# Kernel tuning notes

Measured on AMD Instinct MI355X. Metric: run time of the kernel, lower is better.

## Reference

```python
import jax, jax.numpy as jnp
import numpy as np

N = 50000      # nodes
E = 800000     # edges (avg degree 16)
DIN = 128
DOUT = 64
ALPHA = 0.5    # DirGATConv mixing coefficient
NEG_SLOPE = 0.2  # PyG GATConv default negative_slope


def setup_inputs() -> dict:
    key = jax.random.key(0)
    ks = jax.random.split(key, 12)
    x = jax.random.normal(ks[0], (N, DIN), jnp.float32)
    edge_index = jax.random.randint(ks[1], (2, E), 0, N, dtype=jnp.int64)

    def p(k, shape):
        return jax.random.normal(k, shape, jnp.float32) * 0.05

    return dict(
        x=x,
        edge_index=edge_index,
        W1=p(ks[2], (DIN, DOUT)), att_src1=p(ks[3], (DOUT,)), att_dst1=p(ks[4], (DOUT,)), b1=jnp.zeros((DOUT,), jnp.float32),
        W2=p(ks[5], (DIN, DOUT)), att_src2=p(ks[6], (DOUT,)), att_dst2=p(ks[7], (DOUT,)), b2=jnp.zeros((DOUT,), jnp.float32),
    )


def _gat_conv(x, src, dst, W, a_src, a_dst, b):
    """PyG GATConv with heads=1: linear, per-dst softmax attention, scatter-add."""
    n = x.shape[0]
    loops = jnp.arange(n, dtype=src.dtype)
    src = jnp.concatenate([src, loops])  # add_self_loops=True (PyG default)
    dst = jnp.concatenate([dst, loops])

    xw = x @ W                                # [N, DOUT]
    a_s = xw @ a_src                          # [N]  per-node src attention score
    a_d = xw @ a_dst                          # [N]  per-node dst attention score
    e = jax.nn.leaky_relu(a_s[src] + a_d[dst], NEG_SLOPE)  # [E+N]

    # numerically-stable softmax over edges grouped by destination node
    m = jax.ops.segment_max(e, dst, num_segments=n)
    m = jnp.where(jnp.isfinite(m), m, 0.0)    # nodes w/o in-edges -> safe value
    ex = jnp.exp(e - m[dst])
    denom = jax.ops.segment_sum(ex, dst, num_segments=n)
    coef = ex / (denom[dst] + 1e-16)          # [E+N]

    out = jax.ops.segment_sum(coef[:, None] * xw[src], dst, num_segments=n)
    return out + b


def reference(x, edge_index, W1, att_src1, att_dst1, b1, W2, att_src2, att_dst2, b2):
    src, dst = edge_index[0], edge_index[1]
    out_fwd = _gat_conv(x, src, dst, W1, att_src1, att_dst1, b1)   # src -> dst
    out_rev = _gat_conv(x, dst, src, W2, att_src2, att_dst2, b2)   # dst -> src (transposed edges)
    return (1.0 - ALPHA) * out_fwd + ALPHA * out_rev
```

## Files before the change

kernel.cpp:

```cpp
#include <hip/hip_runtime.h>

#define DIN 128
#define DOUT 64
#define NEG_SLOPE 0.2f
#define ALPHA 0.5f
#define NBUK 512
#define EPB  4096
#define CAP  4608
#define BCCAP 6144

typedef __attribute__((ext_vector_type(8))) short bf16x8;
typedef __attribute__((ext_vector_type(4))) float f32x4;

__device__ __forceinline__ float lrelu(float x) { return x > 0.0f ? x : NEG_SLOPE * x; }

__device__ __forceinline__ unsigned short f2bf(float f) {
    unsigned u = __float_as_uint(f);
    unsigned r = (u + 0x7fffu + ((u >> 16) & 1u)) >> 16;
    return (unsigned short)r;
}
__device__ __forceinline__ float bf2f(unsigned short h) {
    return __uint_as_float((unsigned)h << 16);
}
__device__ __forceinline__ float readlane_f(float v, int l) {
    return __int_as_float(__builtin_amdgcn_readlane(__float_as_int(v), l));
}

__device__ __forceinline__ void dev_wfrag(
    const float* __restrict__ W1, const float* __restrict__ W2,
    unsigned short* __restrict__ wf, int blk, int tid)
{
    int combo = blk * 4 + (tid >> 6);
    int mat = combo >> 4;
    int kk = (combo >> 2) & 3;
    int t = combo & 3;
    int l = tid & 63;
    int g = l >> 4, c = l & 15;
    const float* W = mat ? W2 : W1;
    #pragma unroll
    for (int j = 0; j < 8; ++j) {
        float w = W[(kk * 32 + g * 8 + j) * DOUT + t * 16 + c];
        wf[(size_t)((mat * 16 + kk * 4 + t) * 512) + l * 8 + j] = f2bf(w);
    }
}

__device__ __forceinline__ void dev_proj(
    const float* __restrict__ x, const unsigned short* __restrict__ wf,
    const float* __restrict__ as1, const float* __restrict__ ad1,
    const float* __restrict__ as2, const float* __restrict__ ad2,
    unsigned short* __restrict__ xw1, unsigned short* __restrict__ xw2,
    float* __restrict__ s1, float* __restrict__ d1,
    float* __restrict__ s2, float* __restrict__ d2, int n, int projblk, int tid)
{
    int ntiles = (n + 15) >> 4;
    int tbase = projblk * 8 + (tid >> 6) * 2;
    if (tbase >= ntiles) return;
    int l = tid & 63;
    int g = l >> 4, c = l & 15;

    bf16x8 ah[2][4];
    #pragma unroll
    for (int u = 0; u < 2; ++u) {
        int arow = (tbase + u) * 16 + c;
        if (arow >= n) arow = n - 1;
        const float* xr = x + (size_t)arow * DIN + g * 8;
        #pragma unroll
        for (int kk = 0; kk < 4; ++kk) {
            float4 v0 = *(const float4*)(xr + kk * 32);
            float4 v1 = *(const float4*)(xr + kk * 32 + 4);
            float xv[8] = {v0.x, v0.y, v0.z, v0.w, v1.x, v1.y, v1.z, v1.w};
            #pragma unroll
            for (int j = 0; j < 8; ++j) ah[u][kk][j] = (short)f2bf(xv[j]);
        }
    }

    float vs1[2][4] = {}, vd1[2][4] = {}, vs2[2][4] = {}, vd2[2][4] = {};
    const bf16x8* wfv = (const bf16x8*)wf;

    #pragma unroll
    for (int t = 0; t < 4; ++t) {
        f32x4 C1[2] = {{0.f,0.f,0.f,0.f},{0.f,0.f,0.f,0.f}};
        f32x4 C2[2] = {{0.f,0.f,0.f,0.f},{0.f,0.f,0.f,0.f}};
        #pragma unroll
        for (int kk = 0; kk < 4; ++kk) {
            bf16x8 bh1 = wfv[(size_t)((0 * 16 + kk * 4 + t) * 64) + l];
            bf16x8 bh2 = wfv[(size_t)((1 * 16 + kk * 4 + t) * 64) + l];
            #pragma unroll
            for (int u = 0; u < 2; ++u) {
                C1[u] = __builtin_amdgcn_mfma_f32_16x16x32_bf16(ah[u][kk], bh1, C1[u], 0, 0, 0);
                C2[u] = __builtin_amdgcn_mfma_f32_16x16x32_bf16(ah[u][kk], bh2, C2[u], 0, 0, 0);
            }
        }
        float a1v = as1[t * 16 + c], a2v = ad1[t * 16 + c];
        float a3v = as2[t * 16 + c], a4v = ad2[t * 16 + c];
        #pragma unroll
        for (int u = 0; u < 2; ++u) {
            #pragma unroll
            for (int r = 0; r < 4; ++r) {
                vs1[u][r] = fmaf(C1[u][r], a1v, vs1[u][r]);
                vd1[u][r] = fmaf(C1[u][r], a2v, vd1[u][r]);
                vs2[u][r] = fmaf(C2[u][r], a3v, vs2[u][r]);
                vd2[u][r] = fmaf(C2[u][r], a4v, vd2[u][r]);
                int node = (tbase + u) * 16 + g * 4 + r;
                if (node < n) {
                    xw1[(size_t)node * DOUT + t * 16 + c] = f2bf(C1[u][r]);
                    xw2[(size_t)node * DOUT + t * 16 + c] = f2bf(C2[u][r]);
                }
            }
        }
    }
    #pragma unroll
    for (int off = 1; off < 16; off <<= 1) {
        #pragma unroll
        for (int u = 0; u < 2; ++u) {
            #pragma unroll
            for (int r = 0; r < 4; ++r) {
                vs1[u][r] += __shfl_xor(vs1[u][r], off);
                vd1[u][r] += __shfl_xor(vd1[u][r], off);
                vs2[u][r] += __shfl_xor(vs2[u][r], off);
                vd2[u][r] += __shfl_xor(vd2[u][r], off);
            }
        }
    }
    if (c == 0) {
        #pragma unroll
        for (int u = 0; u < 2; ++u) {
            #pragma unroll
            for (int r = 0; r < 4; ++r) {
                int node = (tbase + u) * 16 + g * 4 + r;
                if (node < n) {
                    s1[node] = vs1[u][r]; d1[node] = vd1[u][r];
                    s2[node] = vs2[u][r]; d2[node] = vd2[u][r];
                }
            }
        }
    }
}

__global__ __launch_bounds__(256) void fusedA_kernel(
    const float* __restrict__ W1, const float* __restrict__ W2,
    unsigned short* __restrict__ wf,
    const int* __restrict__ src, const int* __restrict__ dst,
    int* __restrict__ bkcur, unsigned* __restrict__ staging,
    int e, int n, int nblk)
{
    __shared__ int cnt[NBUK];
    int blk = blockIdx.x, tid = threadIdx.x;
    if (blk >= nblk) { dev_wfrag(W1, W2, wf, blk - nblk, tid); return; }

    for (int b = tid; b < NBUK; b += 256) cnt[b] = 0;
    __syncthreads();
    int base = blk * EPB;
    for (int k = 0; k < EPB / 256; ++k) {
        int t = base + k * 256 + tid;
        if (t < e) {
            atomicAdd(&cnt[dst[t] >> 8], 1);
            atomicAdd(&cnt[(n + src[t]) >> 8], 1);
        }
    }
    __syncthreads();
    for (int b = tid; b < NBUK; b += 256) {
        int c = cnt[b];
        cnt[b] = c ? atomicAdd(&bkcur[b], c) : 0;
    }
    __syncthreads();
    for (int k = 0; k < EPB / 256; ++k) {
        int t = base + k * 256 + tid;
        if (t < e) {
            int s = src[t], d = dst[t];
            int bF = d >> 8;
            int pF = atomicAdd(&cnt[bF], 1);
            if (pF < CAP)
                staging[(size_t)bF * CAP + pF] = ((unsigned)(d & 255) << 16) | (unsigned)s;
            int segR = n + s;
            int bR = segR >> 8;
            int pR = atomicAdd(&cnt[bR], 1);
            if (pR < CAP)
                staging[(size_t)bR * CAP + pR] = ((unsigned)(segR & 255) << 16) | (unsigned)d;
        }
    }
}

__global__ __launch_bounds__(256) void fusedB_kernel(
    const int* __restrict__ bkcur, const unsigned* __restrict__ staging,
    int* __restrict__ csr, int* __restrict__ offs,
    int n2, int e2, int nbuk_eff,
    const float* __restrict__ x, const unsigned short* __restrict__ wf,
    const float* __restrict__ as1, const float* __restrict__ ad1,
    const float* __restrict__ as2, const float* __restrict__ ad2,
    unsigned short* __restrict__ xw1, unsigned short* __restrict__ xw2,
    float* __restrict__ s1, float* __restrict__ d1,
    float* __restrict__ s2, float* __restrict__ d2, int n)
{
    __shared__ int cb[NBUK];
    __shared__ int sc[256];
    __shared__ int segcnt[256];
    __shared__ int segoff[256];
    __shared__ unsigned cache[BCCAP];
    int blk = blockIdx.x, tid = threadIdx.x;
    if (blk >= nbuk_eff) {
        dev_proj(x, wf, as1, ad1, as2, ad2, xw1, xw2, s1, d1, s2, d2, n,
                 blk - nbuk_eff, tid);
        return;
    }
    int b = blk;

    int v0 = bkcur[2 * tid], v1 = bkcur[2 * tid + 1];
    cb[2 * tid] = v0; cb[2 * tid + 1] = v1;
    int pairsum = v0 + v1;
    sc[tid] = pairsum;
    __syncthreads();
    for (int o = 1; o < 256; o <<= 1) {
        int u = (tid >= o) ? sc[tid - o] : 0;
        __syncthreads();
        sc[tid] += u;
        __syncthreads();
    }
    int q = b >> 1;
    int lo = (q > 0 ? sc[q - 1] : 0) + ((b & 1) ? cb[2 * q] : 0);
    int count = cb[b];
    int sbase = b * CAP;

    segcnt[tid] = 0;
    __syncthreads();
    if (count <= BCCAP) {
        for (int k = tid; k < count; k += 256) {
            unsigned st = staging[sbase + k];
            cache[k] = st;
            atomicAdd(&segcnt[st >> 16], 1);
        }
    } else {
        for (int k = tid; k < count; k += 256)
            atomicAdd(&segcnt[staging[sbase + k] >> 16], 1);
    }
    __syncthreads();
    if (tid < 64) {
        int a0 = segcnt[4 * tid], a1 = segcnt[4 * tid + 1];
        int a2 = segcnt[4 * tid + 2], a3 = segcnt[4 * tid + 3];
        int s = a0 + a1 + a2 + a3;
        int inc = s;
        #pragma unroll
        for (int off = 1; off < 64; off <<= 1) {
            int u = __shfl_up(inc, off);
            if (tid >= off) inc += u;
        }
        int excl = inc - s;
        segoff[4 * tid] = excl;
        segoff[4 * tid + 1] = excl + a0;
        segoff[4 * tid + 2] = excl + a0 + a1;
        segoff[4 * tid + 3] = excl + a0 + a1 + a2;
    }
    __syncthreads();
    {
        int seg = (b << 8) + tid;
        if (seg < n2) offs[seg] = lo + segoff[tid];
        segcnt[tid] = segoff[tid];
    }
    if (b == nbuk_eff - 1 && tid == 0) offs[n2] = e2;
    __syncthreads();
    if (count <= BCCAP) {
        for (int k = tid; k < count; k += 256) {
            unsigned st = cache[k];
            int pos = atomicAdd(&segcnt[st >> 16], 1);
            csr[lo + pos] = (int)(st & 0xFFFFu);
        }
    } else {
        for (int k = tid; k < count; k += 256) {
            unsigned st = staging[sbase + k];
            int pos = atomicAdd(&segcnt[st >> 16], 1);
            csr[lo + pos] = (int)(st & 0xFFFFu);
        }
    }
}

__global__ __launch_bounds__(256) void gather_kernel(
    const int* __restrict__ offs, const int* __restrict__ csr,
    const float* __restrict__ s1, const float* __restrict__ d1,
    const float* __restrict__ s2, const float* __restrict__ d2,
    const unsigned short* __restrict__ xw1, const unsigned short* __restrict__ xw2,
    const float* __restrict__ b1, const float* __restrict__ b2,
    float* __restrict__ out, int n)
{
    int i = (blockIdx.x * 256 + threadIdx.x) >> 6;
    int lane = threadIdx.x & 63;
    if (i >= n) return;

    float d1i = d1[i], d2i = d2[i];
    int cF = offs[i],     endF = offs[i + 1];
    int cR = offs[n + i], endR = offs[n + i + 1];

    float pSF = __expf(lrelu(s1[i] + d1i));
    float pSR = __expf(lrelu(s2[i] + d2i));
    float lF0 = pSF, lF1 = 0.f, lR0 = pSR, lR1 = 0.f;
    float aF0 = pSF * bf2f(xw1[(size_t)i * DOUT + lane]), aF1 = 0.f, aF2 = 0.f, aF3 = 0.f;
    float aR0 = pSR * bf2f(xw2[(size_t)i * DOUT + lane]), aR1 = 0.f, aR2 = 0.f, aR3 = 0.f;

    while (cF < endF || cR < endR) {
        int cntF = endF - cF; cntF = cntF < 0 ? 0 : (cntF > 64 ? 64 : cntF);
        int cntR = endR - cR; cntR = cntR < 0 ? 0 : (cntR > 64 ? 64 : cntR);

        int jF = 0, jR = 0;
        float pF = 0.0f, pR = 0.0f;
        if (lane < cntF) { jF = csr[cF + lane]; pF = __expf(lrelu(s1[jF] + d1i)); }
        if (lane < cntR) { jR = csr[cR + lane]; pR = __expf(lrelu(s2[jR] + d2i)); }

        int tmax = cntF > cntR ? cntF : cntR;
        int t = 0;
        for (; t + 4 <= tmax; t += 4) {
            float pF0 = readlane_f(pF, t),     pF1 = readlane_f(pF, t + 1);
            float pF2 = readlane_f(pF, t + 2), pF3 = readlane_f(pF, t + 3);
            int   jF0 = __builtin_amdgcn_readlane(jF, t);
            int   jF1 = __builtin_amdgcn_readlane(jF, t + 1);
            int   jF2 = __builtin_amdgcn_readlane(jF, t + 2);
            int   jF3 = __builtin_amdgcn_readlane(jF, t + 3);
            float pR0 = readlane_f(pR, t),     pR1 = readlane_f(pR, t + 1);
            float pR2 = readlane_f(pR, t + 2), pR3 = readlane_f(pR, t + 3);
            int   jR0 = __builtin_amdgcn_readlane(jR, t);
            int   jR1 = __builtin_amdgcn_readlane(jR, t + 1);
            int   jR2 = __builtin_amdgcn_readlane(jR, t + 2);
            int   jR3 = __builtin_amdgcn_readlane(jR, t + 3);
            lF0 += pF0 + pF1; lF1 += pF2 + pF3;
            lR0 += pR0 + pR1; lR1 += pR2 + pR3;
            aF0 = fmaf(pF0, bf2f(xw1[(size_t)jF0 * DOUT + lane]), aF0);
            aF1 = fmaf(pF1, bf2f(xw1[(size_t)jF1 * DOUT + lane]), aF1);
            aF2 = fmaf(pF2, bf2f(xw1[(size_t)jF2 * DOUT + lane]), aF2);
            aF3 = fmaf(pF3, bf2f(xw1[(size_t)jF3 * DOUT + lane]), aF3);
            aR0 = fmaf(pR0, bf2f(xw2[(size_t)jR0 * DOUT + lane]), aR0);
            aR1 = fmaf(pR1, bf2f(xw2[(size_t)jR1 * DOUT + lane]), aR1);
            aR2 = fmaf(pR2, bf2f(xw2[(size_t)jR2 * DOUT + lane]), aR2);
            aR3 = fmaf(pR3, bf2f(xw2[(size_t)jR3 * DOUT + lane]), aR3);
        }
        for (; t < tmax; ++t) {
            float pF0 = readlane_f(pF, t);
            int   jF0 = __builtin_amdgcn_readlane(jF, t);
            float pR0 = readlane_f(pR, t);
            int   jR0 = __builtin_amdgcn_readlane(jR, t);
            lF0 += pF0; lR0 += pR0;
            aF0 = fmaf(pF0, bf2f(xw1[(size_t)jF0 * DOUT + lane]), aF0);
            aR0 = fmaf(pR0, bf2f(xw2[(size_t)jR0 * DOUT + lane]), aR0);
        }
        cF += cntF;
        cR += cntR;
    }

    float lF = lF0 + lF1, lR = lR0 + lR1;
    float resF = ((aF0 + aF1) + (aF2 + aF3)) / (lF + 1e-16f);
    float resR = ((aR0 + aR1) + (aR2 + aR3)) / (lR + 1e-16f);
    out[(size_t)i * DOUT + lane] =
        (1.0f - ALPHA) * (resF + b1[lane]) + ALPHA * (resR + b2[lane]);
}

extern "C" void kernel_launch(void* const* d_in, const int* in_sizes, int n_in,
                              void* d_out, int out_size, void* d_ws, size_t ws_size,
                              hipStream_t stream) {
    const float* x   = (const float*)d_in[0];
    const int*   ei  = (const int*)d_in[1];
    const float* W1  = (const float*)d_in[2];
    const float* as1 = (const float*)d_in[3];
    const float* ad1 = (const float*)d_in[4];
    const float* b1  = (const float*)d_in[5];
    const float* W2  = (const float*)d_in[6];
    const float* as2 = (const float*)d_in[7];
    const float* ad2 = (const float*)d_in[8];
    const float* b2  = (const float*)d_in[9];
    float* out = (float*)d_out;

    int n = in_sizes[0] / DIN;
    int e = in_sizes[1] / 2;
    const int* src = ei;
    const int* dst = ei + e;
    int n2 = 2 * n;
    int e2 = 2 * e;
    int nblk = (e + EPB - 1) / EPB;
    int nbuk_eff = (n2 + 255) >> 8;
    int ntiles16 = (n + 15) >> 4;
    int projblks = (ntiles16 + 7) / 8;

    unsigned short* xw1 = (unsigned short*)d_ws;
    unsigned short* xw2 = xw1 + (size_t)n * DOUT;
    float* s1  = (float*)(xw2 + (size_t)n * DOUT);
    float* d1  = s1 + n;
    float* s2  = d1 + n;
    float* d2  = s2 + n;
    unsigned short* wf = (unsigned short*)(d2 + n);
    int* bkcur = (int*)(wf + 16384);
    int* offs  = bkcur + NBUK;
    int* csr   = offs + (size_t)n2 + 1;
    unsigned* staging = (unsigned*)(csr + (size_t)e2);

    hipMemsetAsync(bkcur, 0, NBUK * sizeof(int), stream);

    fusedA_kernel<<<nblk + 8, 256, 0, stream>>>(W1, W2, wf, src, dst,
                                                bkcur, staging, e, n, nblk);

    fusedB_kernel<<<nbuk_eff + projblks, 256, 0, stream>>>(
        bkcur, staging, csr, offs, n2, e2, nbuk_eff,
        x, wf, as1, ad1, as2, ad2, xw1, xw2, s1, d1, s2, d2, n);

    long long gthreads = (long long)n * 64;
    int gblocks = (int)((gthreads + 255) / 256);
    gather_kernel<<<gblocks, 256, 0, stream>>>(offs, csr, s1, d1, s2, d2,
                                               xw1, xw2, b1, b2, out, n);
}
```

Baseline: 101.0 us.

## Unroll gather by eight, cache edges in LDS, use packed bf16 converts

```diff
diff --git a/kernel.cpp b/kernel.cpp
--- a/kernel.cpp
+++ b/kernel.cpp
@@ -21,6 +21,11 @@
 }
 __device__ __forceinline__ float bf2f(unsigned short h) {
     return __uint_as_float((unsigned)h << 16);
+}
+__device__ __forceinline__ unsigned cvt_pk_bf16(float a, float b) {
+    unsigned r;
+    asm("v_cvt_pk_bf16_f32 %0, %1, %2" : "=v"(r) : "v"(a), "v"(b));
+    return r;
 }
 __device__ __forceinline__ float readlane_f(float v, int l) {
     return __int_as_float(__builtin_amdgcn_readlane(__float_as_int(v), l));
@@ -68,9 +73,11 @@
         for (int kk = 0; kk < 4; ++kk) {
             float4 v0 = *(const float4*)(xr + kk * 32);
             float4 v1 = *(const float4*)(xr + kk * 32 + 4);
-            float xv[8] = {v0.x, v0.y, v0.z, v0.w, v1.x, v1.y, v1.z, v1.w};
-            #pragma unroll
-            for (int j = 0; j < 8; ++j) ah[u][kk][j] = (short)f2bf(xv[j]);
+            unsigned* dw = (unsigned*)&ah[u][kk];
+            dw[0] = cvt_pk_bf16(v0.x, v0.y);
+            dw[1] = cvt_pk_bf16(v0.z, v0.w);
+            dw[2] = cvt_pk_bf16(v1.x, v1.y);
+            dw[3] = cvt_pk_bf16(v1.z, v1.w);
         }
     }
 
@@ -101,10 +108,21 @@
                 vd1[u][r] = fmaf(C1[u][r], a2v, vd1[u][r]);
                 vs2[u][r] = fmaf(C2[u][r], a3v, vs2[u][r]);
                 vd2[u][r] = fmaf(C2[u][r], a4v, vd2[u][r]);
+            }
+            unsigned w1a = cvt_pk_bf16(C1[u][0], C1[u][1]);
+            unsigned w1b = cvt_pk_bf16(C1[u][2], C1[u][3]);
+            unsigned w2a = cvt_pk_bf16(C2[u][0], C2[u][1]);
+            unsigned w2b = cvt_pk_bf16(C2[u][2], C2[u][3]);
+            unsigned short v1s[4] = {(unsigned short)w1a, (unsigned short)(w1a >> 16),
+                                     (unsigned short)w1b, (unsigned short)(w1b >> 16)};
+            unsigned short v2s[4] = {(unsigned short)w2a, (unsigned short)(w2a >> 16),
+                                     (unsigned short)w2b, (unsigned short)(w2b >> 16)};
+            #pragma unroll
+            for (int r = 0; r < 4; ++r) {
                 int node = (tbase + u) * 16 + g * 4 + r;
                 if (node < n) {
-                    xw1[(size_t)node * DOUT + t * 16 + c] = f2bf(C1[u][r]);
-                    xw2[(size_t)node * DOUT + t * 16 + c] = f2bf(C2[u][r]);
+                    xw1[(size_t)node * DOUT + t * 16 + c] = v1s[r];
+                    xw2[(size_t)node * DOUT + t * 16 + c] = v2s[r];
                 }
             }
         }
@@ -145,6 +163,8 @@
     int e, int n, int nblk)
 {
     __shared__ int cnt[NBUK];
+    __shared__ int es[EPB];
+    __shared__ int ed[EPB];
     int blk = blockIdx.x, tid = threadIdx.x;
     if (blk >= nblk) { dev_wfrag(W1, W2, wf, blk - nblk, tid); return; }
 
@@ -152,11 +172,15 @@
     __syncthreads();
     int base = blk * EPB;
     for (int k = 0; k < EPB / 256; ++k) {
-        int t = base + k * 256 + tid;
+        int li = k * 256 + tid;
+        int t = base + li;
+        int s = -1, d = -1;
         if (t < e) {
-            atomicAdd(&cnt[dst[t] >> 8], 1);
-            atomicAdd(&cnt[(n + src[t]) >> 8], 1);
-        }
+            s = src[t]; d = dst[t];
+            atomicAdd(&cnt[d >> 8], 1);
+            atomicAdd(&cnt[(n + s) >> 8], 1);
+        }
+        es[li] = s; ed[li] = d;
     }
     __syncthreads();
     for (int b = tid; b < NBUK; b += 256) {
@@ -165,9 +189,9 @@
     }
     __syncthreads();
     for (int k = 0; k < EPB / 256; ++k) {
-        int t = base + k * 256 + tid;
-        if (t < e) {
-            int s = src[t], d = dst[t];
+        int li = k * 256 + tid;
+        int s = es[li], d = ed[li];
+        if (s >= 0) {
             int bF = d >> 8;
             int pF = atomicAdd(&cnt[bF], 1);
             if (pF < CAP)
@@ -291,9 +315,10 @@
 
     float pSF = __expf(lrelu(s1[i] + d1i));
     float pSR = __expf(lrelu(s2[i] + d2i));
-    float lF0 = pSF, lF1 = 0.f, lR0 = pSR, lR1 = 0.f;
-    float aF0 = pSF * bf2f(xw1[(size_t)i * DOUT + lane]), aF1 = 0.f, aF2 = 0.f, aF3 = 0.f;
-    float aR0 = pSR * bf2f(xw2[(size_t)i * DOUT + lane]), aR1 = 0.f, aR2 = 0.f, aR3 = 0.f;
+    float lFa = pSF, lFb = 0.f, lRa = pSR, lRb = 0.f;
+    float aF[8] = {}, aR[8] = {};
+    aF[0] = pSF * bf2f(xw1[(size_t)i * DOUT + lane]);
+    aR[0] = pSR * bf2f(xw2[(size_t)i * DOUT + lane]);
 
     while (cF < endF || cR < endR) {
         int cntF = endF - cF; cntF = cntF < 0 ? 0 : (cntF > 64 ? 64 : cntF);
@@ -305,47 +330,41 @@
         if (lane < cntR) { jR = csr[cR + lane]; pR = __expf(lrelu(s2[jR] + d2i)); }
 
         int tmax = cntF > cntR ? cntF : cntR;
-        int t = 0;
-        for (; t + 4 <= tmax; t += 4) {
-            float pF0 = readlane_f(pF, t),     pF1 = readlane_f(pF, t + 1);
-            float pF2 = readlane_f(pF, t + 2), pF3 = readlane_f(pF, t + 3);
-            int   jF0 = __builtin_amdgcn_readlane(jF, t);
-            int   jF1 = __builtin_amdgcn_readlane(jF, t + 1);
-            int   jF2 = __builtin_amdgcn_readlane(jF, t + 2);
-            int   jF3 = __builtin_amdgcn_readlane(jF, t + 3);
-            float pR0 = readlane_f(pR, t),     pR1 = readlane_f(pR, t + 1);
-            float pR2 = readlane_f(pR, t + 2), pR3 = readlane_f(pR, t + 3);
-            int   jR0 = __builtin_amdgcn_readlane(jR, t);
-            int   jR1 = __builtin_amdgcn_readlane(jR, t + 1);
-            int   jR2 = __builtin_amdgcn_readlane(jR, t + 2);
-            int   jR3 = __builtin_amdgcn_readlane(jR, t + 3);
-            lF0 += pF0 + pF1; lF1 += pF2 + pF3;
-            lR0 += pR0 + pR1; lR1 += pR2 + pR3;
-            aF0 = fmaf(pF0, bf2f(xw1[(size_t)jF0 * DOUT + lane]), aF0);
-            aF1 = fmaf(pF1, bf2f(xw1[(size_t)jF1 * DOUT + lane]), aF1);
-            aF2 = fmaf(pF2, bf2f(xw1[(size_t)jF2 * DOUT + lane]), aF2);
-            aF3 = fmaf(pF3, bf2f(xw1[(size_t)jF3 * DOUT + lane]), aF3);
-            aR0 = fmaf(pR0, bf2f(xw2[(size_t)jR0 * DOUT + lane]), aR0);
-            aR1 = fmaf(pR1, bf2f(xw2[(size_t)jR1 * DOUT + lane]), aR1);
-            aR2 = fmaf(pR2, bf2f(xw2[(size_t)jR2 * DOUT + lane]), aR2);
-            aR3 = fmaf(pR3, bf2f(xw2[(size_t)jR3 * DOUT + lane]), aR3);
-        }
-        for (; t < tmax; ++t) {
-            float pF0 = readlane_f(pF, t);
-            int   jF0 = __builtin_amdgcn_readlane(jF, t);
-            float pR0 = readlane_f(pR, t);
-            int   jR0 = __builtin_amdgcn_readlane(jR, t);
-            lF0 += pF0; lR0 += pR0;
-            aF0 = fmaf(pF0, bf2f(xw1[(size_t)jF0 * DOUT + lane]), aF0);
-            aR0 = fmaf(pR0, bf2f(xw2[(size_t)jR0 * DOUT + lane]), aR0);
+        int tmax8 = (tmax + 7) & ~7;
+        for (int t = 0; t < tmax8; t += 8) {
+            float pFs[8], pRs[8]; int jFs[8], jRs[8];
+            #pragma unroll
+            for (int u = 0; u < 8; ++u) {
+                pFs[u] = readlane_f(pF, t + u);
+                jFs[u] = __builtin_amdgcn_readlane(jF, t + u);
+                pRs[u] = readlane_f(pR, t + u);
+                jRs[u] = __builtin_amdgcn_readlane(jR, t + u);
+            }
+            float vF[8], vR[8];
+            #pragma unroll
+            for (int u = 0; u < 8; ++u) {
+                vF[u] = bf2f(xw1[(size_t)jFs[u] * DOUT + lane]);
+                vR[u] = bf2f(xw2[(size_t)jRs[u] * DOUT + lane]);
+            }
+            #pragma unroll
+            for (int u = 0; u < 8; ++u) {
+                aF[u] = fmaf(pFs[u], vF[u], aF[u]);
+                aR[u] = fmaf(pRs[u], vR[u], aR[u]);
+            }
+            lFa += (pFs[0] + pFs[1]) + (pFs[2] + pFs[3]);
+            lFb += (pFs[4] + pFs[5]) + (pFs[6] + pFs[7]);
+            lRa += (pRs[0] + pRs[1]) + (pRs[2] + pRs[3]);
+            lRb += (pRs[4] + pRs[5]) + (pRs[6] + pRs[7]);
         }
         cF += cntF;
         cR += cntR;
     }
 
-    float lF = lF0 + lF1, lR = lR0 + lR1;
-    float resF = ((aF0 + aF1) + (aF2 + aF3)) / (lF + 1e-16f);
-    float resR = ((aR0 + aR1) + (aR2 + aR3)) / (lR + 1e-16f);
+    float lF = lFa + lFb, lR = lRa + lRb;
+    float sF = ((aF[0] + aF[1]) + (aF[2] + aF[3])) + ((aF[4] + aF[5]) + (aF[6] + aF[7]));
+    float sR = ((aR[0] + aR[1]) + (aR[2] + aR[3])) + ((aR[4] + aR[5]) + (aR[6] + aR[7]));
+    float resF = sF / (lF + 1e-16f);
+    float resR = sR / (lR + 1e-16f);
     out[(size_t)i * DOUT + lane] =
         (1.0f - ALPHA) * (resF + b1[lane]) + ALPHA * (resR + b2[lane]);
 }
```

Result: faster. 97.69 us (-3.3%).
